# Optimization experiments

Measured on AMD Instinct MI355X. Metric: run time of the kernel, lower is better.

## Reference

```python
import jax, jax.numpy as jnp
import numpy as np

N, E, G = 4096, 16384, 16
IN_C, EDGE_C, H = 3, 4, 128
LN_EPS = 1e-5


def setup_inputs() -> dict:
    key = jax.random.key(0)
    ks = jax.random.split(key, 32)
    nrm = lambda k, shp, s: jax.random.normal(k, shp, jnp.float32) * s
    inp = {}
    inp["x"] = nrm(ks[0], (N, IN_C), 1.0)
    inp["edge_index"] = jax.random.randint(ks[1], (2, E), 0, N)
    inp["edge_attr"] = nrm(ks[2], (E, EDGE_C), 1.0)
    inp["batch"] = jnp.sort(jax.random.randint(ks[3], (N,), 0, G))
    inp["contingency_type"] = nrm(ks[4], (G, 4), 1.0)
    inp["load_scale"] = nrm(ks[5], (G,), 1.0)
    i = 6
    def conv_params(prefix, in_c):
        nonlocal i
        inp[prefix + "_w1"] = nrm(ks[i], (EDGE_C, 128), 1.0 / np.sqrt(EDGE_C)); i += 1
        inp[prefix + "_b1"] = jnp.zeros((128,), jnp.float32)
        inp[prefix + "_w2"] = nrm(ks[i], (128, in_c * H), 1.0 / np.sqrt(128)); i += 1
        inp[prefix + "_b2"] = jnp.zeros((in_c * H,), jnp.float32)
        inp[prefix + "_root"] = nrm(ks[i], (in_c, H), 1.0 / np.sqrt(in_c)); i += 1
        inp[prefix + "_bias"] = jnp.zeros((H,), jnp.float32)
    conv_params("c1", IN_C)
    conv_params("c2", H)
    conv_params("c3", H)
    for p in ("ln1", "ln2", "ln3"):
        inp[p + "_g"] = jnp.ones((H,), jnp.float32)
        inp[p + "_b"] = jnp.zeros((H,), jnp.float32)
    inp["lin_w"] = nrm(ks[i], (2 * H + 4 + 1, 2), 1.0 / np.sqrt(2 * H + 5)); i += 1
    inp["lin_b"] = jnp.zeros((2,), jnp.float32)
    return inp


def _nnconv(x, src, dst, edge_attr, w1, b1, w2, b2, root, bias, in_c):
    # edge MLP -> per-edge weight matrix [E, in_c, H]
    h = jax.nn.relu(edge_attr @ w1 + b1)
    W = (h @ w2 + b2).reshape(-1, in_c, H)
    msg = jnp.einsum('ei,eio->eo', x[src], W)  # gather + per-edge matmul
    s = jax.ops.segment_sum(msg, dst, num_segments=N)
    cnt = jax.ops.segment_sum(jnp.ones((msg.shape[0],), msg.dtype), dst, num_segments=N)
    agg = s / jnp.maximum(cnt, 1.0)[:, None]  # scatter-mean
    return agg + x @ root + bias


def _layernorm(x, g, b):
    m = jnp.mean(x, axis=-1, keepdims=True)
    v = jnp.mean(jnp.square(x - m), axis=-1, keepdims=True)
    return (x - m) * jax.lax.rsqrt(v + LN_EPS) * g + b


def reference(x, edge_index, edge_attr, batch, contingency_type, load_scale,
              c1_w1, c1_b1, c1_w2, c1_b2, c1_root, c1_bias,
              c2_w1, c2_b1, c2_w2, c2_b2, c2_root, c2_bias,
              c3_w1, c3_b1, c3_w2, c3_b2, c3_root, c3_bias,
              ln1_g, ln1_b, ln2_g, ln2_b, ln3_g, ln3_b,
              lin_w, lin_b):
    src, dst = edge_index[0], edge_index[1]
    h = _nnconv(x, src, dst, edge_attr, c1_w1, c1_b1, c1_w2, c1_b2, c1_root, c1_bias, IN_C)
    h = jax.nn.relu(_layernorm(h, ln1_g, ln1_b))
    h = _nnconv(h, src, dst, edge_attr, c2_w1, c2_b1, c2_w2, c2_b2, c2_root, c2_bias, H)
    h = jax.nn.elu(_layernorm(h, ln2_g, ln2_b))
    h = _nnconv(h, src, dst, edge_attr, c3_w1, c3_b1, c3_w2, c3_b2, c3_root, c3_bias, H)
    h = jax.nn.leaky_relu(_layernorm(h, ln3_g, ln3_b), negative_slope=0.01)
    # global mean / max pool over graphs
    gsum = jax.ops.segment_sum(h, batch, num_segments=G)
    gcnt = jax.ops.segment_sum(jnp.ones((N,), h.dtype), batch, num_segments=G)
    gmean = gsum / jnp.maximum(gcnt, 1.0)[:, None]
    gmax = jax.ops.segment_max(h, batch, num_segments=G)
    gmax = jnp.where(gcnt[:, None] > 0, gmax, 0.0)
    x_cat = jnp.concatenate([gmean, gmax, contingency_type, load_scale[:, None]], axis=1)
    return x_cat @ lin_w + lin_b
```

## Files before the change

### kernel.cpp

```cpp
#include <hip/hip_runtime.h>
#include <hip/hip_bf16.h>


#define N_NODES 4096
#define N_EDGES 16384
#define N_GRAPHS 16
#define HD 128
#define BM 128
#define LDB 136
#define KSPLIT 2
#define KT_PER (HD / KSPLIT)
#define SLAB_E (HD * HD)

typedef unsigned short ushort_t;
typedef __attribute__((ext_vector_type(8))) short short8;
typedef __attribute__((ext_vector_type(4))) float f32x4;

static __device__ __forceinline__ ushort_t f2b(float f) {
    __hip_bfloat16 h = __float2bfloat16(f);
    union { __hip_bfloat16 h; ushort_t u; } cv; cv.h = h; return cv.u;
}
static __device__ __forceinline__ float b2f(ushort_t u) {
    union { unsigned u; float f; } cv; cv.u = ((unsigned)u) << 16; return cv.f;
}

static __device__ __forceinline__ float wave_sum(float v) {
#pragma unroll
    for (int off = 1; off < 64; off <<= 1) v += __shfl_xor(v, off, 64);
    return v;
}

__global__ __launch_bounds__(256) void prep1(
    const int* __restrict__ src, const int* __restrict__ dst, const float* __restrict__ x,
    float* __restrict__ cnt, float* __restrict__ sfeat,
    const float* __restrict__ w2, ushort_t* __restrict__ w2r) {
    __shared__ ushort_t tile[HD][LDB];
    const int b = blockIdx.x;
    const int t = threadIdx.x;
    if (b < N_EDGES / 256) {
        int e = b * 256 + t;
        int d = dst[e], s = src[e];
        atomicAdd(&cnt[d], 1.0f);
        atomicAdd(&sfeat[d * 4 + 0], x[s * 3 + 0]);
        atomicAdd(&sfeat[d * 4 + 1], x[s * 3 + 1]);
        atomicAdd(&sfeat[d * 4 + 2], x[s * 3 + 2]);
    } else {
        const int i = b - N_EDGES / 256;
        for (int c = 0; c < 64; ++c) {
            int flat = c * 256 + t;
            int k = flat >> 7, o = flat & 127;
            tile[o][k] = f2b(w2[k * 384 + i * HD + o]);
        }
        __syncthreads();
        uint4* outp = (uint4*)(w2r + (size_t)i * SLAB_E);
        for (int it = 0; it < 8; ++it) {
            int c = it * 256 + t;
            int ng = c >> 9, j = (c >> 6) & 7, l = c & 63;
            int ni = j >> 2, kb = j & 3;
            int R  = ng * 32 + ni * 16 + (l & 15);
            int ke = kb * 32 + (l >> 4) * 8;
            outp[c] = *(const uint4*)&tile[R][ke];
        }
    }
}

__global__ __launch_bounds__(512, 2) void l1_gemm(
    const float* __restrict__ x, const int* __restrict__ src, const int* __restrict__ dst,
    const float* __restrict__ ea, const float* __restrict__ w1, const float* __restrict__ b1,
    const ushort_t* __restrict__ w2r, float* __restrict__ agg) {
    __shared__ ushort_t Hs[SLAB_E];
    __shared__ float    XV[3][BM];

    const int t = threadIdx.x;
    const int lane = t & 63, quad = lane >> 4, l16 = lane & 15;
    const int wave = t >> 6;
    const int mg = wave >> 2;
    const int ng = wave & 3;
    const int e0 = blockIdx.x * BM;
    const int rbase = mg * 64;

    {
        const int e = t & 127;
        const int kb32 = (t >> 7) * 32;
        const float4 av = ((const float4*)ea)[e0 + e];
        if (t < 128) {
            const int n = src[e0 + t];
            XV[0][t] = x[n * 3 + 0]; XV[1][t] = x[n * 3 + 1]; XV[2][t] = x[n * 3 + 2];
        }
        const int r7 = e & 7;
        ushort_t* hrow = Hs + e * HD;
#pragma unroll
        for (int c = 0; c < 4; ++c) {
            const int kbase = kb32 + c * 8;
            unsigned pk0, pk1, pk2, pk3;
#pragma unroll
            for (int u = 0; u < 4; ++u) {
                const int ka = kbase + 2 * u, kb = ka + 1;
                float s0 = b1[ka];
                s0 = fmaf(av.x, w1[0 * HD + ka], s0);
                s0 = fmaf(av.y, w1[1 * HD + ka], s0);
                s0 = fmaf(av.z, w1[2 * HD + ka], s0);
                s0 = fmaf(av.w, w1[3 * HD + ka], s0);
                float s1 = b1[kb];
                s1 = fmaf(av.x, w1[0 * HD + kb], s1);
                s1 = fmaf(av.y, w1[1 * HD + kb], s1);
                s1 = fmaf(av.z, w1[2 * HD + kb], s1);
                s1 = fmaf(av.w, w1[3 * HD + kb], s1);
                unsigned pr = (unsigned)f2b(fmaxf(s0, 0.0f)) |
                              ((unsigned)f2b(fmaxf(s1, 0.0f)) << 16);
                if (u == 0) pk0 = pr; else if (u == 1) pk1 = pr;
                else if (u == 2) pk2 = pr; else pk3 = pr;
            }
            uint4 v; v.x = pk0; v.y = pk1; v.z = pk2; v.w = pk3;
            *(uint4*)&hrow[(((kbase >> 3) ^ r7) << 3)] = v;
        }
    }
    __syncthreads();

    short8 afrag[4][4];
#pragma unroll
    for (int mi = 0; mi < 4; ++mi) {
        const int R = rbase + mi * 16 + l16;
        const ushort_t* rowp = Hs + R * HD;
        const int r7 = R & 7;
#pragma unroll
        for (int kb = 0; kb < 4; ++kb)
            afrag[mi][kb] = *(const short8*)&rowp[((kb * 4 + quad) ^ r7) << 3];
    }

    f32x4 acc[4][2];
#pragma unroll
    for (int mi = 0; mi < 4; ++mi)
#pragma unroll
        for (int ni = 0; ni < 2; ++ni)
            acc[mi][ni] = (f32x4){0.f, 0.f, 0.f, 0.f};

    const ushort_t* bbase = w2r + (size_t)ng * 4096 + (size_t)lane * 8;

#define LOADB(bf, slab)                                                         \
    {                                                                           \
        const ushort_t* bw = bbase + (size_t)(slab) * SLAB_E;                   \
        _Pragma("unroll") for (int ni = 0; ni < 2; ++ni)                        \
            _Pragma("unroll") for (int kb = 0; kb < 4; ++kb)                    \
                bf[ni][kb] = *(const short8*)(bw + (ni * 4 + kb) * 512);        \
    }
#define CONSUME_XV(bf, i)                                                       \
    {                                                                           \
        _Pragma("unroll") for (int mi = 0; mi < 4; ++mi) {                      \
            float4 xv = *(const float4*)&XV[i][rbase + mi * 16 + quad * 4];     \
            _Pragma("unroll") for (int ni = 0; ni < 2; ++ni) {                  \
                f32x4 p = {0.f, 0.f, 0.f, 0.f};                                 \
                _Pragma("unroll") for (int kb = 0; kb < 4; ++kb)                \
                    p = __builtin_amdgcn_mfma_f32_16x16x32_bf16(                \
                        afrag[mi][kb], bf[ni][kb], p, 0, 0, 0);                 \
                acc[mi][ni][0] = fmaf(xv.x, p[0], acc[mi][ni][0]);              \
                acc[mi][ni][1] = fmaf(xv.y, p[1], acc[mi][ni][1]);              \
                acc[mi][ni][2] = fmaf(xv.z, p[2], acc[mi][ni][2]);              \
                acc[mi][ni][3] = fmaf(xv.w, p[3], acc[mi][ni][3]);              \
            }                                                                   \
        }                                                                       \
    }

    short8 bfA[2][4], bfB[2][4];
    LOADB(bfA, 0);
    LOADB(bfB, 1);
    CONSUME_XV(bfA, 0);
    LOADB(bfA, 2);
    CONSUME_XV(bfB, 1);
    CONSUME_XV(bfA, 2);
#undef LOADB
#undef CONSUME_XV

#pragma unroll
    for (int mi = 0; mi < 4; ++mi) {
#pragma unroll
        for (int r = 0; r < 4; ++r) {
            const int dn = dst[e0 + rbase + mi * 16 + quad * 4 + r];
#pragma unroll
            for (int ni = 0; ni < 2; ++ni)
                atomicAdd(&agg[dn * HD + ng * 32 + ni * 16 + l16], acc[mi][ni][r]);
        }
    }
}

__global__ __launch_bounds__(128) void node_update_l1(
    float* __restrict__ agg, const float* __restrict__ cnt, const float* __restrict__ sfeat,
    const float* __restrict__ x, const float* __restrict__ root, const float* __restrict__ bias,
    const float* __restrict__ b2, const float* __restrict__ lng, const float* __restrict__ lnb) {
    const int n = blockIdx.x, o = threadIdx.x;
    float s = bias[o];
#pragma unroll
    for (int i = 0; i < 3; ++i) s = fmaf(x[n * 3 + i], root[i * HD + o], s);
    float sb = 0.0f;
#pragma unroll
    for (int i = 0; i < 3; ++i) sb = fmaf(sfeat[n * 4 + i], b2[i * HD + o], sb);
    float v = (agg[n * HD + o] + sb) / fmaxf(cnt[n], 1.0f) + s;
    __shared__ float red[2];
    float ws = wave_sum(v);
    if ((o & 63) == 0) red[o >> 6] = ws;
    __syncthreads();
    float m = (red[0] + red[1]) * (1.0f / HD);
    float d = v - m;
    float ws2 = wave_sum(d * d);
    __syncthreads();
    if ((o & 63) == 0) red[o >> 6] = ws2;
    __syncthreads();
    float var = (red[0] + red[1]) * (1.0f / HD);
    float y = d * rsqrtf(var + 1e-5f) * lng[o] + lnb[o];
    agg[n * HD + o] = fmaxf(y, 0.0f);
}

__global__ __launch_bounds__(256) void w2t_prep(const float* __restrict__ w2,
                                                const float* __restrict__ b2,
                                                ushort_t* __restrict__ w2t) {
    __shared__ ushort_t tile[HD][LDB];
    const int kt = blockIdx.x;
    const int t = threadIdx.x;
    const float* srcp = (kt < HD) ? (w2 + kt * HD * HD) : b2;
    for (int c = 0; c < 64; ++c) {
        int flat = c * 256 + t;
        int i = flat >> 7, o = flat & 127;
        tile[o][i] = f2b(srcp[i * HD + o]);
    }
    __syncthreads();
    uint4* outp = (uint4*)(w2t + (size_t)kt * SLAB_E);
    for (int it = 0; it < 8; ++it) {
        int c = it * 256 + t;
        int ng = c >> 9, j = (c >> 6) & 7, l = c & 63;
        int ni = j >> 2, kb = j & 3;
        int R  = ng * 32 + ni * 16 + (l & 15);
        int ke = kb * 32 + (l >> 4) * 8;
        outp[c] = *(const uint4*)&tile[R][ke];
    }
}

__global__ __launch_bounds__(512, 2) void gemm_mfma(
    const float* __restrict__ hprev, const float* __restrict__ ea,
    const float* __restrict__ w1, const float* __restrict__ b1,
    const ushort_t* __restrict__ w2t,
    const int* __restrict__ src, const int* __restrict__ dst,
    float* __restrict__ agg) {
    __shared__ ushort_t Xs[SLAB_E];
    __shared__ ushort_t HeT[KT_PER][BM];

    const int t = threadIdx.x;
    const int lane = t & 63, quad = lane >> 4, l16 = lane & 15;
    const int wave = t >> 6;
    const int mg = wave >> 2;
    const int ng = wave & 3;
    const int eb = blockIdx.x >> 1;
    const int ks = blockIdx.x & 1;
    const int k0 = ks * KT_PER;
    const int e0 = eb * BM;
    const int rbase = mg * 64;

    {
        const int le = t >> 2;
        const int j0 = (t & 3) * 4;
        const int r7 = le & 7;
        const float* rp = hprev + src[e0 + le] * HD + (t & 3) * 32;
        ushort_t* xrow = Xs + le * HD;
#pragma unroll
        for (int c = 0; c < 4; ++c) {
            float4 va = ((const float4*)rp)[2 * c];
            float4 vb = ((const float4*)rp)[2 * c + 1];
            uint4 pk;
            pk.x = (unsigned)f2b(va.x) | ((unsigned)f2b(va.y) << 16);
            pk.y = (unsigned)f2b(va.z) | ((unsigned)f2b(va.w) << 16);
            pk.z = (unsigned)f2b(vb.x) | ((unsigned)f2b(vb.y) << 16);
            pk.w = (unsigned)f2b(vb.z) | ((unsigned)f2b(vb.w) << 16);
            *(uint4*)&xrow[((j0 + c) ^ r7) << 3] = pk;
        }
    }

    {
        const int e = t & 127;
        const float4 av = ((const float4*)ea)[e0 + e];
        for (int kl = t >> 7; kl < KT_PER; kl += 4) {
            const int kt = k0 + kl;
            float s = b1[kt];
            s = fmaf(av.x, w1[0 * HD + kt], s);
            s = fmaf(av.y, w1[1 * HD + kt], s);
            s = fmaf(av.z, w1[2 * HD + kt], s);
            s = fmaf(av.w, w1[3 * HD + kt], s);
            HeT[kl][e] = f2b(fmaxf(s, 0.0f));
        }
    }
    __syncthreads();

    short8 afrag[4][4];
#pragma unroll
    for (int mi = 0; mi < 4; ++mi) {
        const int R = rbase + mi * 16 + l16;
        const ushort_t* rowp = Xs + R * HD;
        const int r7 = R & 7;
#pragma unroll
        for (int kb = 0; kb < 4; ++kb)
            afrag[mi][kb] = *(const short8*)&rowp[((kb * 4 + quad) ^ r7) << 3];
    }

    f32x4 acc[4][2];
#pragma unroll
    for (int mi = 0; mi < 4; ++mi)
#pragma unroll
        for (int ni = 0; ni < 2; ++ni)
            acc[mi][ni] = (f32x4){0.f, 0.f, 0.f, 0.f};

    const ushort_t* bbase = w2t + (size_t)ng * 4096 + (size_t)lane * 8;

#define LOADB(bf, slab)                                                         \
    {                                                                           \
        const ushort_t* bw = bbase + (size_t)(slab) * SLAB_E;                   \
        _Pragma("unroll") for (int ni = 0; ni < 2; ++ni)                        \
            _Pragma("unroll") for (int kb = 0; kb < 4; ++kb)                    \
                bf[ni][kb] = *(const short8*)(bw + (ni * 4 + kb) * 512);        \
    }
#define CONSUME(bf, s)                                                          \
    {                                                                           \
        _Pragma("unroll") for (int mi = 0; mi < 4; ++mi) {                      \
            ushort4 hv = *(const ushort4*)&HeT[s][rbase + mi * 16 + quad * 4];  \
            float h0 = b2f(hv.x), h1 = b2f(hv.y), h2 = b2f(hv.z), h3 = b2f(hv.w);\
            _Pragma("unroll") for (int ni = 0; ni < 2; ++ni) {                  \
                f32x4 p = {0.f, 0.f, 0.f, 0.f};                                 \
                _Pragma("unroll") for (int kb = 0; kb < 4; ++kb)                \
                    p = __builtin_amdgcn_mfma_f32_16x16x32_bf16(                \
                        afrag[mi][kb], bf[ni][kb], p, 0, 0, 0);                 \
                acc[mi][ni][0] = fmaf(h0, p[0], acc[mi][ni][0]);                \
                acc[mi][ni][1] = fmaf(h1, p[1], acc[mi][ni][1]);                \
                acc[mi][ni][2] = fmaf(h2, p[2], acc[mi][ni][2]);                \
                acc[mi][ni][3] = fmaf(h3, p[3], acc[mi][ni][3]);                \
            }                                                                   \
        }                                                                       \
    }

    short8 bfA[2][4], bfB[2][4];
    LOADB(bfA, k0);
    for (int s = 0; s < KT_PER; s += 2) {
        LOADB(bfB, k0 + s + 1);
        CONSUME(bfA, s);
        __builtin_amdgcn_s_barrier();
        if (s + 2 < KT_PER) LOADB(bfA, k0 + s + 2)
        else if (ks == 1)   LOADB(bfA, HD);
        CONSUME(bfB, s + 1);
        __builtin_amdgcn_s_barrier();
    }
    if (ks == 1) {
#pragma unroll
        for (int mi = 0; mi < 4; ++mi)
#pragma unroll
            for (int ni = 0; ni < 2; ++ni) {
                f32x4 p = {0.f, 0.f, 0.f, 0.f};
#pragma unroll
                for (int kb = 0; kb < 4; ++kb)
                    p = __builtin_amdgcn_mfma_f32_16x16x32_bf16(
                        afrag[mi][kb], bfA[ni][kb], p, 0, 0, 0);
                acc[mi][ni][0] += p[0]; acc[mi][ni][1] += p[1];
                acc[mi][ni][2] += p[2]; acc[mi][ni][3] += p[3];
            }
    }
#undef LOADB
#undef CONSUME

#pragma unroll
    for (int mi = 0; mi < 4; ++mi) {
#pragma unroll
        for (int r = 0; r < 4; ++r) {
            const int dn = dst[e0 + rbase + mi * 16 + quad * 4 + r];
#pragma unroll
            for (int ni = 0; ni < 2; ++ni)
                atomicAdd(&agg[dn * HD + ng * 32 + ni * 16 + l16], acc[mi][ni][r]);
        }
    }
}

__global__ __launch_bounds__(128) void node_update(
    float* __restrict__ agg, const float* __restrict__ cnt,
    float* __restrict__ hprev, const float* __restrict__ root, const float* __restrict__ bias,
    const float* __restrict__ lng, const float* __restrict__ lnb) {
    const int n = blockIdx.x, o = threadIdx.x;
    __shared__ float hr[HD];
    hr[o] = hprev[n * HD + o];
    __syncthreads();
    float s = bias[o];
#pragma unroll 8
    for (int k = 0; k < HD; ++k) s = fmaf(hr[k], root[k * HD + o], s);
    float v = agg[n * HD + o] / fmaxf(cnt[n], 1.0f) + s;
    __shared__ float red[2];
    float ws = wave_sum(v);
    if ((o & 63) == 0) red[o >> 6] = ws;
    __syncthreads();
    float m = (red[0] + red[1]) * (1.0f / HD);
    float d = v - m;
    float ws2 = wave_sum(d * d);
    __syncthreads();
    if ((o & 63) == 0) red[o >> 6] = ws2;
    __syncthreads();
    float var = (red[0] + red[1]) * (1.0f / HD);
    float y = d * rsqrtf(var + 1e-5f) * lng[o] + lnb[o];
    y = (y > 0.0f) ? y : expm1f(y);
    agg[n * HD + o] = y;
    hprev[n * HD + o] = 0.0f;
}

static __device__ __forceinline__ unsigned fkey(float f) {
    unsigned b = __float_as_uint(f);
    return (b & 0x80000000u) ? ~b : (b | 0x80000000u);
}
__global__ __launch_bounds__(128) void node_update_pool(
    const float* __restrict__ agg, const float* __restrict__ cnt,
    const float* __restrict__ hprev, const float* __restrict__ root, const float* __restrict__ bias,
    const float* __restrict__ lng, const float* __restrict__ lnb,
    const int* __restrict__ batch,
    float* __restrict__ gsum, unsigned* __restrict__ gmaxk, int* __restrict__ gcnt) {
    const int n = blockIdx.x, o = threadIdx.x;
    __shared__ float hr[HD];
    hr[o] = hprev[n * HD + o];
    __syncthreads();
    float s = bias[o];
#pragma unroll 8
    for (int k = 0; k < HD; ++k) s = fmaf(hr[k], root[k * HD + o], s);
    float v = agg[n * HD + o] / fmaxf(cnt[n], 1.0f) + s;
    __shared__ float red[2];
    float ws = wave_sum(v);
    if ((o & 63) == 0) red[o >> 6] = ws;
    __syncthreads();
    float m = (red[0] + red[1]) * (1.0f / HD);
    float d = v - m;
    float ws2 = wave_sum(d * d);
    __syncthreads();
    if ((o & 63) == 0) red[o >> 6] = ws2;
    __syncthreads();
    float var = (red[0] + red[1]) * (1.0f / HD);
    float y = d * rsqrtf(var + 1e-5f) * lng[o] + lnb[o];
    y = (y > 0.0f) ? y : 0.01f * y;
    const int g = batch[n];
    atomicAdd(&gsum[g * HD + o], y);
    atomicMax(&gmaxk[g * HD + o], fkey(y));
    if (o == 0) atomicAdd(&gcnt[g], 1);
}

__global__ __launch_bounds__(128) void pool_head2(
    const float* __restrict__ gsum, const unsigned* __restrict__ gmaxk, const int* __restrict__ gcnt,
    const float* __restrict__ cont, const float* __restrict__ ls,
    const float* __restrict__ lin_w, const float* __restrict__ lin_b, float* __restrict__ out) {
    const int g = blockIdx.x, o = threadIdx.x;
    const int c = gcnt[g];
    __shared__ float xcat[2 * HD + 5];
    xcat[o] = gsum[g * HD + o] / fmaxf((float)c, 1.0f);
    unsigned key = gmaxk[g * HD + o];
    unsigned bits = (key & 0x80000000u) ? (key & 0x7FFFFFFFu) : ~key;
    xcat[HD + o] = (c > 0) ? __uint_as_float(bits) : 0.0f;
    if (o < 4) xcat[2 * HD + o] = cont[g * 4 + o];
    if (o == 0) xcat[2 * HD + 4] = ls[g];
    __syncthreads();
    if (o < 2) {
        float r = lin_b[o];
        for (int ri = 0; ri < 2 * HD + 5; ++ri) r = fmaf(xcat[ri], lin_w[ri * 2 + o], r);
        out[g * 2 + o] = r;
    }
}

extern "C" void kernel_launch(void* const* d_in, const int* in_sizes, int n_in,
                              void* d_out, int out_size, void* d_ws, size_t ws_size,
                              hipStream_t stream) {
    const float* x     = (const float*)d_in[0];
    const int*   ei    = (const int*)d_in[1];
    const float* ea    = (const float*)d_in[2];
    const int*   batch = (const int*)d_in[3];
    const float* cont  = (const float*)d_in[4];
    const float* ls    = (const float*)d_in[5];
    const float *c1_w1 = (const float*)d_in[6],  *c1_b1 = (const float*)d_in[7];
    const float *c1_w2 = (const float*)d_in[8],  *c1_b2 = (const float*)d_in[9];
    const float *c1_rt = (const float*)d_in[10], *c1_bs = (const float*)d_in[11];
    const float *c2_w1 = (const float*)d_in[12], *c2_b1 = (const float*)d_in[13];
    const float *c2_w2 = (const float*)d_in[14], *c2_b2 = (const float*)d_in[15];
    const float *c2_rt = (const float*)d_in[16], *c2_bs = (const float*)d_in[17];
    const float *c3_w1 = (const float*)d_in[18], *c3_b1 = (const float*)d_in[19];
    const float *c3_w2 = (const float*)d_in[20], *c3_b2 = (const float*)d_in[21];
    const float *c3_rt = (const float*)d_in[22], *c3_bs = (const float*)d_in[23];
    const float *ln1g = (const float*)d_in[24], *ln1b = (const float*)d_in[25];
    const float *ln2g = (const float*)d_in[26], *ln2b = (const float*)d_in[27];
    const float *ln3g = (const float*)d_in[28], *ln3b = (const float*)d_in[29];
    const float *lin_w = (const float*)d_in[30], *lin_b = (const float*)d_in[31];
    float* out = (float*)d_out;

    float*    cnt   = (float*)d_ws;
    float*    sfeat = cnt + N_NODES;
    float*    bufA  = sfeat + 4 * N_NODES;
    float*    bufB  = bufA + N_NODES * HD;
    ushort_t* w2t   = (ushort_t*)(bufB + N_NODES * HD);
    float*    gsum  = (float*)(w2t + (HD + 1) * HD * HD);
    unsigned* gmaxk = (unsigned*)(gsum + N_GRAPHS * HD);
    int*      gcnt  = (int*)(gmaxk + N_GRAPHS * HD);
    const int* src = ei;
    const int* dst = ei + N_EDGES;

    size_t ws_bytes = (size_t)((char*)(gcnt + N_GRAPHS) - (char*)d_ws);
    hipMemsetAsync(d_ws, 0, ws_bytes, stream);

    prep1<<<N_EDGES / 256 + 3, 256, 0, stream>>>(src, dst, x, cnt, sfeat, c1_w2, w2t);

    l1_gemm<<<N_EDGES / BM, 512, 0, stream>>>(x, src, dst, ea, c1_w1, c1_b1, w2t, bufA);
    node_update_l1<<<N_NODES, 128, 0, stream>>>(bufA, cnt, sfeat, x, c1_rt, c1_bs, c1_b2, ln1g, ln1b);

    w2t_prep<<<HD + 1, 256, 0, stream>>>(c2_w2, c2_b2, w2t);
    gemm_mfma<<<(N_EDGES / BM) * KSPLIT, 512, 0, stream>>>(bufA, ea, c2_w1, c2_b1, w2t, src, dst, bufB);
    node_update<<<N_NODES, 128, 0, stream>>>(bufB, cnt, bufA, c2_rt, c2_bs, ln2g, ln2b);

    w2t_prep<<<HD + 1, 256, 0, stream>>>(c3_w2, c3_b2, w2t);
    gemm_mfma<<<(N_EDGES / BM) * KSPLIT, 512, 0, stream>>>(bufB, ea, c3_w1, c3_b1, w2t, src, dst, bufA);
    node_update_pool<<<N_NODES, 128, 0, stream>>>(bufA, cnt, bufB, c3_rt, c3_bs, ln3g, ln3b,
                                                  batch, gsum, gmaxk, gcnt);

    pool_head2<<<N_GRAPHS, 128, 0, stream>>>(gsum, gmaxk, gcnt, cont, ls, lin_w, lin_b, out);
}
```

Measured before the change: 390.0 us.

## Split edge GEMM K dimension four ways and reload A fragments per step

Raises the K-split of the per-edge MFMA GEMM from 2 to 4, so twice as many blocks each handle a quarter of the edge-MLP hidden units. The A fragments are reloaded from LDS at every step instead of being held in registers, and the B double-buffering is removed, which cuts register pressure at the cost of more LDS reads and less latency hiding. The weight transpose-prep kernel now uses 1024 threads per block. More blocks means the gather of node features is repeated per split and more atomic adds are issued to the aggregation buffer.

Result: slower. 414.4 us (+6.2%).

```diff
diff --git a/kernel.cpp b/kernel.cpp
--- a/kernel.cpp
+++ b/kernel.cpp
@@ -8,7 +8,7 @@
 #define HD 128
 #define BM 128
 #define LDB 136
-#define KSPLIT 2
+#define KSPLIT 4
 #define KT_PER (HD / KSPLIT)
 #define SLAB_E (HD * HD)
 
@@ -210,22 +210,22 @@
     agg[n * HD + o] = fmaxf(y, 0.0f);
 }
 
-__global__ __launch_bounds__(256) void w2t_prep(const float* __restrict__ w2,
-                                                const float* __restrict__ b2,
-                                                ushort_t* __restrict__ w2t) {
+__global__ __launch_bounds__(1024) void w2t_prep(const float* __restrict__ w2,
+                                                 const float* __restrict__ b2,
+                                                 ushort_t* __restrict__ w2t) {
     __shared__ ushort_t tile[HD][LDB];
     const int kt = blockIdx.x;
     const int t = threadIdx.x;
     const float* srcp = (kt < HD) ? (w2 + kt * HD * HD) : b2;
-    for (int c = 0; c < 64; ++c) {
-        int flat = c * 256 + t;
+    for (int c = 0; c < 16; ++c) {
+        int flat = c * 1024 + t;
         int i = flat >> 7, o = flat & 127;
         tile[o][i] = f2b(srcp[i * HD + o]);
     }
     __syncthreads();
     uint4* outp = (uint4*)(w2t + (size_t)kt * SLAB_E);
-    for (int it = 0; it < 8; ++it) {
-        int c = it * 256 + t;
+    for (int it = 0; it < 2; ++it) {
+        int c = it * 1024 + t;
         int ng = c >> 9, j = (c >> 6) & 7, l = c & 63;
         int ni = j >> 2, kb = j & 3;
         int R  = ng * 32 + ni * 16 + (l & 15);
@@ -248,8 +248,8 @@
     const int wave = t >> 6;
     const int mg = wave >> 2;
     const int ng = wave & 3;
-    const int eb = blockIdx.x >> 1;
-    const int ks = blockIdx.x & 1;
+    const int eb = blockIdx.x >> 2;
+    const int ks = blockIdx.x & 3;
     const int k0 = ks * KT_PER;
     const int e0 = eb * BM;
     const int rbase = mg * 64;
@@ -288,17 +288,6 @@
     }
     __syncthreads();
 
-    short8 afrag[4][4];
-#pragma unroll
-    for (int mi = 0; mi < 4; ++mi) {
-        const int R = rbase + mi * 16 + l16;
-        const ushort_t* rowp = Xs + R * HD;
-        const int r7 = R & 7;
-#pragma unroll
-        for (int kb = 0; kb < 4; ++kb)
-            afrag[mi][kb] = *(const short8*)&rowp[((kb * 4 + quad) ^ r7) << 3];
-    }
-
     f32x4 acc[4][2];
 #pragma unroll
     for (int mi = 0; mi < 4; ++mi)
@@ -318,13 +307,19 @@
 #define CONSUME(bf, s)                                                          \
     {                                                                           \
         _Pragma("unroll") for (int mi = 0; mi < 4; ++mi) {                      \
+            const int R = rbase + mi * 16 + l16;                                \
+            const ushort_t* rowp = Xs + R * HD;                                 \
+            const int r7 = R & 7;                                               \
+            short8 af[4];                                                       \
+            _Pragma("unroll") for (int kb = 0; kb < 4; ++kb)                    \
+                af[kb] = *(const short8*)&rowp[((kb * 4 + quad) ^ r7) << 3];    \
             ushort4 hv = *(const ushort4*)&HeT[s][rbase + mi * 16 + quad * 4];  \
             float h0 = b2f(hv.x), h1 = b2f(hv.y), h2 = b2f(hv.z), h3 = b2f(hv.w);\
             _Pragma("unroll") for (int ni = 0; ni < 2; ++ni) {                  \
                 f32x4 p = {0.f, 0.f, 0.f, 0.f};                                 \
                 _Pragma("unroll") for (int kb = 0; kb < 4; ++kb)                \
                     p = __builtin_amdgcn_mfma_f32_16x16x32_bf16(                \
-                        afrag[mi][kb], bf[ni][kb], p, 0, 0, 0);                 \
+                        af[kb], bf[ni][kb], p, 0, 0, 0);                        \
                 acc[mi][ni][0] = fmaf(h0, p[0], acc[mi][ni][0]);                \
                 acc[mi][ni][1] = fmaf(h1, p[1], acc[mi][ni][1]);                \
                 acc[mi][ni][2] = fmaf(h2, p[2], acc[mi][ni][2]);                \
@@ -333,30 +328,34 @@
         }                                                                       \
     }
 
-    short8 bfA[2][4], bfB[2][4];
-    LOADB(bfA, k0);
-    for (int s = 0; s < KT_PER; s += 2) {
-        LOADB(bfB, k0 + s + 1);
-        CONSUME(bfA, s);
+    short8 bf[2][4];
+    for (int s = 0; s < KT_PER; ++s) {
+        LOADB(bf, k0 + s);
+        CONSUME(bf, s);
         __builtin_amdgcn_s_barrier();
-        if (s + 2 < KT_PER) LOADB(bfA, k0 + s + 2)
-        else if (ks == 1)   LOADB(bfA, HD);
-        CONSUME(bfB, s + 1);
-        __builtin_amdgcn_s_barrier();
-    }
-    if (ks == 1) {
-#pragma unroll
-        for (int mi = 0; mi < 4; ++mi)
+    }
+    if (ks == KSPLIT - 1) {
+        LOADB(bf, HD);
+#pragma unroll
+        for (int mi = 0; mi < 4; ++mi) {
+            const int R = rbase + mi * 16 + l16;
+            const ushort_t* rowp = Xs + R * HD;
+            const int r7 = R & 7;
+            short8 af[4];
+#pragma unroll
+            for (int kb = 0; kb < 4; ++kb)
+                af[kb] = *(const short8*)&rowp[((kb * 4 + quad) ^ r7) << 3];
 #pragma unroll
             for (int ni = 0; ni < 2; ++ni) {
                 f32x4 p = {0.f, 0.f, 0.f, 0.f};
 #pragma unroll
                 for (int kb = 0; kb < 4; ++kb)
                     p = __builtin_amdgcn_mfma_f32_16x16x32_bf16(
-                        afrag[mi][kb], bfA[ni][kb], p, 0, 0, 0);
+                        af[kb], bf[ni][kb], p, 0, 0, 0);
                 acc[mi][ni][0] += p[0]; acc[mi][ni][1] += p[1];
                 acc[mi][ni][2] += p[2]; acc[mi][ni][3] += p[3];
             }
+        }
     }
 #undef LOADB
 #undef CONSUME
@@ -503,11 +502,11 @@
     l1_gemm<<<N_EDGES / BM, 512, 0, stream>>>(x, src, dst, ea, c1_w1, c1_b1, w2t, bufA);
     node_update_l1<<<N_NODES, 128, 0, stream>>>(bufA, cnt, sfeat, x, c1_rt, c1_bs, c1_b2, ln1g, ln1b);
 
-    w2t_prep<<<HD + 1, 256, 0, stream>>>(c2_w2, c2_b2, w2t);
+    w2t_prep<<<HD + 1, 1024, 0, stream>>>(c2_w2, c2_b2, w2t);
     gemm_mfma<<<(N_EDGES / BM) * KSPLIT, 512, 0, stream>>>(bufA, ea, c2_w1, c2_b1, w2t, src, dst, bufB);
     node_update<<<N_NODES, 128, 0, stream>>>(bufB, cnt, bufA, c2_rt, c2_bs, ln2g, ln2b);
 
-    w2t_prep<<<HD + 1, 256, 0, stream>>>(c3_w2, c3_b2, w2t);
+    w2t_prep<<<HD + 1, 1024, 0, stream>>>(c3_w2, c3_b2, w2t);
     gemm_mfma<<<(N_EDGES / BM) * KSPLIT, 512, 0, stream>>>(bufB, ea, c3_w1, c3_b1, w2t, src, dst, bufA);
     node_update_pool<<<N_NODES, 128, 0, stream>>>(bufA, cnt, bufB, c3_rt, c3_bs, ln3g, ln3b,
                                                   batch, gsum, gmaxk, gcnt);
```
